# Performance work log

Hardware: AMD Instinct MI355X
Metric: run time of the kernel (lower is better)

Reference implementation:

```python
import jax, jax.numpy as jnp
import numpy as np

B, N, D, K = 4, 8192, 128, 16


def setup_inputs() -> dict:
    key = jax.random.key(0)
    ks = jax.random.split(key, 12)
    w = lambda k, s: (jax.random.normal(k, s, jnp.float32) * 0.02)
    return {
        "xyz": jax.random.normal(ks[0], (B, N, 3), jnp.float32),
        "feat": jax.random.normal(ks[1], (B, N, D), jnp.float32),
        # Linear weights stored as (in, out); apply as x @ W + b
        "Wq": w(ks[2], (D, D)), "bq": jnp.zeros((D,), jnp.float32),
        "Wk": w(ks[3], (D, D)), "bk": jnp.zeros((D,), jnp.float32),
        "Wv": w(ks[4], (D, D)), "bv": jnp.zeros((D,), jnp.float32),
        "Wp1": w(ks[5], (3, D)), "bp1": jnp.zeros((D,), jnp.float32),
        "Wp2": w(ks[6], (D, D)), "bp2": jnp.zeros((D,), jnp.float32),
        "Wo": w(ks[7], (D, D)), "bo": jnp.zeros((D,), jnp.float32),
        "gamma": jnp.float32(0.5),
    }


def reference(xyz, feat, Wq, bq, Wk, bk, Wv, bv, Wp1, bp1, Wp2, bp2, Wo, bo, gamma):
    # pairwise squared distance (B,N,N)
    sq = jnp.sum(xyz * xyz, axis=-1)
    dist = sq[:, :, None] + sq[:, None, :] - 2.0 * jnp.einsum("bnc,bmc->bnm", xyz, xyz)
    # K nearest neighbors (smallest distance)
    _, idx = jax.lax.top_k(-dist, K)  # (B,N,K)
    bidx = jnp.arange(B)[:, None, None]
    n_xyz = xyz[bidx, idx]    # (B,N,K,3)
    n_feat = feat[bidx, idx]  # (B,N,K,D)

    q = (feat @ Wq + bq)[:, :, None, :]    # (B,N,1,D)
    kk = n_feat @ Wk + bk                  # (B,N,K,D)
    v = n_feat @ Wv + bv                   # (B,N,K,D)

    rel_pos = xyz[:, :, None, :] - n_xyz   # (B,N,K,3)
    pos_enc = jax.nn.relu(rel_pos @ Wp1 + bp1) @ Wp2 + bp2  # (B,N,K,D)

    # per-channel-summed attention score, softmax over neighbor axis
    score = jnp.sum(q - kk + pos_enc, axis=-1, keepdims=True)  # (B,N,K,1)
    attn = jax.nn.softmax(score, axis=-2)

    agg = jnp.sum(attn * (v + pos_enc), axis=2)  # (B,N,D)
    out = agg @ Wo + bo
    return feat + gamma * out
```

## Files before the change

### kernel.cpp

```cpp
#include <hip/hip_runtime.h>
#include <hip/hip_bf16.h>

#define BATCH 4
#define NPTS  8192
#define DIM   128
#define KNN   16
#define NROWS (BATCH * NPTS)

#define SPLITS 16
#define RANGE  512
#define TILE   256
#define DEPTH  32
#define DEPTHP 34
#define NSUB   8

using u64  = unsigned long long;
using u32  = unsigned int;

__device__ __forceinline__ unsigned short f2bf(float f) {
    u32 u = __float_as_uint(f);
    u32 r = (u + 0x7FFFu + ((u >> 16) & 1u)) >> 16;
    return (unsigned short)r;
}
__device__ __forceinline__ u32 fordkey(float f) {
    u32 u = __float_as_uint(f);
    return (u & 0x80000000u) ? ~u : (u | 0x80000000u);
}
__device__ __forceinline__ float invkey(u32 k) {
    u32 u = (k & 0x80000000u) ? (k & 0x7FFFFFFFu) : ~k;
    return __uint_as_float(u);
}

__device__ __forceinline__ void insert16(u64 key, u64* ks) {
    if (key < ks[15]) {
#pragma unroll
        for (int t = 0; t < 16; ++t) {
            u64 lo = key < ks[t] ? key : ks[t];
            u64 hi = key < ks[t] ? ks[t] : key;
            ks[t] = lo;
            key = hi;
        }
    }
}

__device__ __forceinline__ float pdist(float4 me, float4 c) {
    float dot = __fadd_rn(__fadd_rn(__fmul_rn(me.x, c.x), __fmul_rn(me.y, c.y)),
                          __fmul_rn(me.z, c.z));
    return __fsub_rn(__fadd_rn(me.w, c.w), __fmul_rn(2.0f, dot));
}

__global__ __launch_bounds__(256) void prep_weights(const float* __restrict__ Wk,
                                                    const float* __restrict__ Wp2,
                                                    float* __restrict__ wk,
                                                    float* __restrict__ w2) {
    int tid = threadIdx.x;
    int c = tid & 127;
    const float* src = (tid < 128) ? Wk : Wp2;
    float s = 0.f;
    for (int d = 0; d < DIM; ++d) s += src[c * DIM + d];
    if (tid < 128) wk[c] = s;
    else           w2[c] = s;
}

__global__ __launch_bounds__(256) void conv_weights(const float* __restrict__ Wv,
                                                    const float* __restrict__ Wp2,
                                                    const float* __restrict__ Wo,
                                                    u32* __restrict__ Wb) {
    int i = blockIdx.x * 256 + threadIdx.x;
    int which = i >> 13, off = i & 8191;
    const float* W = (which == 0) ? Wv : (which == 1 ? Wp2 : Wo);
    float2 w = ((const float2*)W)[off];
    Wb[i] = (u32)f2bf(w.x) | ((u32)f2bf(w.y) << 16);
}

__global__ __launch_bounds__(256) void prep_points(const float* __restrict__ xyz,
                                                   const float* __restrict__ feat,
                                                   const float* __restrict__ wk,
                                                   float4* __restrict__ pts,
                                                   float* __restrict__ sK) {
    int lid = threadIdx.x & 63;
    int p = blockIdx.x * 4 + (threadIdx.x >> 6);
    float f_lo = feat[(size_t)p * DIM + lid];
    float f_hi = feat[(size_t)p * DIM + 64 + lid];
    float s = fmaf(f_lo, wk[lid], f_hi * wk[64 + lid]);
#pragma unroll
    for (int m = 32; m >= 1; m >>= 1) s += __shfl_xor(s, m);
    if (lid == 0) {
        float x = xyz[p * 3 + 0];
        float y = xyz[p * 3 + 1];
        float z = xyz[p * 3 + 2];
        float sq = __fadd_rn(__fadd_rn(__fmul_rn(x, x), __fmul_rn(y, y)), __fmul_rn(z, z));
        pts[p] = make_float4(x, y, z, sq);
        sK[p] = s;
    }
}

__global__ __launch_bounds__(256) void knn_limpass(const float4* __restrict__ pts,
                                                   float* __restrict__ dlim) {
    __shared__ float4 tile[256];
    __shared__ unsigned short stk[4][64][DEPTHP];
    int y = blockIdx.y;
    int wavein = threadIdx.x >> 6, lane = threadIdx.x & 63;
    int q = blockIdx.x * 256 + wavein * 64 + lane;
    int b = q >> 13;
    float4 me = pts[q];
    {
        float4 c = pts[b * NPTS + y * 256 + threadIdx.x];
        tile[threadIdx.x] = make_float4(c.x, c.y, c.z, -0.5f * c.w);
    }
    __syncthreads();
    float ks[16];
#pragma unroll
    for (int t = 0; t < 16; ++t) ks[t] = INFINITY;
    unsigned short* mystk = stk[wavein][lane];

    for (int jj = 0; jj < 32; ++jj) {
        float4 c = tile[jj];
        float s = fmaf(me.x, c.x, fmaf(me.y, c.y, fmaf(me.z, c.z, c.w)));
        float d = fmaf(-2.0f, s, me.w);
        if (d < ks[15]) {
#pragma unroll
            for (int t = 0; t < 16; ++t) {
                float lo = fminf(d, ks[t]);
                float hi = fmaxf(d, ks[t]);
                ks[t] = lo;
                d = hi;
            }
        }
    }
    float lim = ks[15];
    for (int c0 = 32; c0 < 256; c0 += 32) {
        int cnt = 0;
#pragma unroll
        for (int jj = c0; jj < c0 + 32; ++jj) {
            float4 c = tile[jj];
            float s = fmaf(me.x, c.x, fmaf(me.y, c.y, fmaf(me.z, c.z, c.w)));
            float d = fmaf(-2.0f, s, me.w);
            int slot = cnt < (DEPTH - 1) ? cnt : (DEPTH - 1);
            mystk[slot] = (unsigned short)jj;
            cnt += (d < lim) ? 1 : 0;
        }
        for (int i = 0; i < cnt; ++i) {
            int jj = mystk[i];
            float4 c = tile[jj];
            float s = fmaf(me.x, c.x, fmaf(me.y, c.y, fmaf(me.z, c.z, c.w)));
            float d = fmaf(-2.0f, s, me.w);
            if (d < ks[15]) {
#pragma unroll
                for (int t = 0; t < 16; ++t) {
                    float lo = fminf(d, ks[t]);
                    float hi = fmaxf(d, ks[t]);
                    ks[t] = lo;
                    d = hi;
                }
            }
        }
        lim = ks[15];
    }
    dlim[(size_t)y * NROWS + q] = ks[15];
}

__global__ __launch_bounds__(256) void knn_partial(const float4* __restrict__ pts,
                                                   const float* __restrict__ dlim,
                                                   unsigned short* __restrict__ part16) {
    __shared__ float4 tile[TILE];
    __shared__ unsigned short stk[4][64][DEPTHP];
    int r = blockIdx.y;
    int wavein = threadIdx.x >> 6, lane = threadIdx.x & 63;
    int q = blockIdx.x * 256 + wavein * 64 + lane;
    int b = q >> 13;
    float4 me = pts[q];

    float T = dlim[q];
#pragma unroll
    for (int y = 1; y < NSUB; ++y) T = fminf(T, dlim[(size_t)y * NROWS + q]);
    float gate_d = T + 2.0e-4f;
    u64 sent = ((u64)fordkey(gate_d) << 32) | 0xFFFFFFFFull;
    u64 ks[16];
#pragma unroll
    for (int t = 0; t < 16; ++t) ks[t] = sent;
    float A = 0.5f * (me.w - gate_d) - 1.0e-4f;
    unsigned short* mystk = stk[wavein][lane];

    for (int tb = 0; tb < RANGE / TILE; ++tb) {
        __syncthreads();
        int jb = r * RANGE + tb * TILE;
        {
            float4 c = pts[b * NPTS + jb + threadIdx.x];
            tile[threadIdx.x] = make_float4(c.x, c.y, c.z, -0.5f * c.w);
        }
        __syncthreads();

        int cnt = 0;
#pragma unroll 4
        for (int jj = 0; jj < TILE; ++jj) {
            float4 c = tile[jj];
            float s = fmaf(me.x, c.x, fmaf(me.y, c.y, fmaf(me.z, c.z, c.w)));
            int slot = cnt < (DEPTH - 1) ? cnt : (DEPTH - 1);
            mystk[slot] = (unsigned short)jj;
            cnt += (s >= A) ? 1 : 0;
        }
        bool over = (cnt >= DEPTH);
        int dn = over ? 0 : cnt;
        for (int i = 0; i < dn; ++i) {
            int jj = mystk[i];
            float4 c = tile[jj];
            float4 cc = make_float4(c.x, c.y, c.z, -2.0f * c.w);
            float d = pdist(me, cc);
            u64 key = ((u64)fordkey(d) << 32) | (u32)(jb + jj);
            insert16(key, ks);
        }
        if (__any(over)) {
            if (over) {
                for (int jj = 0; jj < TILE; ++jj) {
                    float4 c = tile[jj];
                    float s = fmaf(me.x, c.x, fmaf(me.y, c.y, fmaf(me.z, c.z, c.w)));
                    if (s >= A) {
                        float4 cc = make_float4(c.x, c.y, c.z, -2.0f * c.w);
                        float d = pdist(me, cc);
                        u64 key = ((u64)fordkey(d) << 32) | (u32)(jb + jj);
                        insert16(key, ks);
                    }
                }
            }
        }
        float nl = invkey((u32)(ks[15] >> 32)) + 1.0e-4f;
        gate_d = (nl < gate_d) ? nl : gate_d;
        A = 0.5f * (me.w - gate_d) - 1.0e-4f;
    }
    u32* dst = (u32*)(part16 + (size_t)q * 256 + r * 16);
#pragma unroll
    for (int t = 0; t < 8; ++t)
        dst[t] = (u32)(ks[2 * t] & 0xFFFFu) | ((u32)(ks[2 * t + 1] & 0xFFFFu) << 16);
}

__global__ __launch_bounds__(256) void knn_merge(const float4* __restrict__ pts,
                                                 const unsigned short* __restrict__ part16,
                                                 int* __restrict__ idx16) {
    int wavein = threadIdx.x >> 6, lane = threadIdx.x & 63;
    int q = blockIdx.x * 4 + wavein;
    int b = q >> 13;
    float4 me = pts[q];
    ushort4 e = *(const ushort4*)(part16 + (size_t)q * 256 + lane * 4);
    u64 k0, k1, k2, k3;
    {
        u32 id;
        id = e.x; k0 = (id != 0xFFFFu) ? (((u64)fordkey(pdist(me, pts[b * NPTS + id])) << 32) | id) : ~0ull;
        id = e.y; k1 = (id != 0xFFFFu) ? (((u64)fordkey(pdist(me, pts[b * NPTS + id])) << 32) | id) : ~0ull;
        id = e.z; k2 = (id != 0xFFFFu) ? (((u64)fordkey(pdist(me, pts[b * NPTS + id])) << 32) | id) : ~0ull;
        id = e.w; k3 = (id != 0xFFFFu) ? (((u64)fordkey(pdist(me, pts[b * NPTS + id])) << 32) | id) : ~0ull;
    }
    u64 t;
    if (k1 < k0) { t = k0; k0 = k1; k1 = t; }
    if (k3 < k2) { t = k2; k2 = k3; k3 = t; }
    if (k2 < k0) { t = k0; k0 = k2; k2 = t; }
    if (k3 < k1) { t = k1; k1 = k3; k3 = t; }
    if (k2 < k1) { t = k1; k1 = k2; k2 = t; }

    u64 cur = k0;
    int head = 0;
    u64 got = 0;
#pragma unroll
    for (int it = 0; it < 16; ++it) {
        u64 m = cur;
#pragma unroll
        for (int s = 32; s >= 1; s >>= 1) {
            u64 o = __shfl_xor(m, s);
            m = (o < m) ? o : m;
        }
        if (m == cur) {
            head++;
            cur = (head == 1) ? k1 : (head == 2) ? k2 : (head == 3) ? k3 : ~0ull;
        }
        if (lane == it) got = m;
    }
    if (lane < 16) idx16[q * KNN + lane] = (int)(got & 0xFFFFFFFFu);
}

template <int MODE>
__global__ __launch_bounds__(256) void gemm32(const float* __restrict__ X,
                                              const u32* __restrict__ Wb,
                                              const float* __restrict__ bias,
                                              const float* __restrict__ add,
                                              const float* __restrict__ featb,
                                              const float* __restrict__ gammap,
                                              float* __restrict__ outv) {
    __shared__ u32 Ws[DIM * DIM / 2];
    __shared__ float Xs[8 * DIM];
    __shared__ float bs[DIM];
    int tid = threadIdx.x;
    {
        const uint4* src = (const uint4*)Wb;
        uint4* dst = (uint4*)Ws;
        for (int i = tid; i < DIM * DIM / 8; i += 256) dst[i] = src[i];
    }
    if (tid < 128) bs[tid] = bias[tid];
    float gamma = 0.f;
    if (MODE == 2) gamma = *gammap;

    int rowBase = blockIdx.x * 32;
    int d4 = (tid & 31) * 4;
    int row = tid >> 5;

    for (int it = 0; it < 4; ++it) {
        int r0 = rowBase + it * 8;
        __syncthreads();
        ((float4*)Xs)[tid] = ((const float4*)(X + (size_t)r0 * DIM))[tid];
        __syncthreads();

        float a0 = bs[d4], a1 = bs[d4 + 1], a2 = bs[d4 + 2], a3 = bs[d4 + 3];
        const float* xr = &Xs[row * DIM];
#pragma unroll 8
        for (int c = 0; c < DIM; ++c) {
            float x = xr[c];
            uint2 w = *(const uint2*)&Ws[c * (DIM / 2) + (d4 >> 1)];
            a0 = fmaf(x, __uint_as_float(w.x << 16), a0);
            a1 = fmaf(x, __uint_as_float(w.x & 0xFFFF0000u), a1);
            a2 = fmaf(x, __uint_as_float(w.y << 16), a2);
            a3 = fmaf(x, __uint_as_float(w.y & 0xFFFF0000u), a3);
        }
        size_t off = (size_t)(r0 + row) * DIM + d4;
        if (MODE == 1) {
            float4 ad = *(const float4*)(add + off);
            a0 += ad.x; a1 += ad.y; a2 += ad.z; a3 += ad.w;
        }
        if (MODE == 2) {
            float4 fb = *(const float4*)(featb + off);
            a0 = fmaf(gamma, a0, fb.x);
            a1 = fmaf(gamma, a1, fb.y);
            a2 = fmaf(gamma, a2, fb.z);
            a3 = fmaf(gamma, a3, fb.w);
        }
        *(float4*)(outv + off) = make_float4(a0, a1, a2, a3);
    }
}

__global__ __launch_bounds__(256) void stage_c(const float4* __restrict__ pts,
                                               const int* __restrict__ idx16,
                                               const float* __restrict__ sK,
                                               const float* __restrict__ w2,
                                               const float* __restrict__ Wp1,
                                               const float* __restrict__ bp1,
                                               const float* __restrict__ Vf,
                                               float* __restrict__ vagg,
                                               float* __restrict__ hbar) {
    __shared__ float hs[4][KNN * DIM];
    int wavein = threadIdx.x >> 6;
    int lid = threadIdx.x & 63;
    int p = blockIdx.x * 4 + wavein;
    int b = p >> 13;
    float4 me = pts[p];

    float wx_lo = Wp1[lid],        wx_hi = Wp1[64 + lid];
    float wy_lo = Wp1[128 + lid],  wy_hi = Wp1[192 + lid];
    float wz_lo = Wp1[256 + lid],  wz_hi = Wp1[320 + lid];
    float bl    = bp1[lid],        bh    = bp1[64 + lid];
    float w2l   = w2[lid],         w2h   = w2[64 + lid];

    int myidx = idx16[p * KNN + (lid & 15)];
    float* h = hs[wavein];
    float sc = -INFINITY;

    for (int k = 0; k < KNN; ++k) {
        int j = __shfl(myidx, k);
        int g = b * NPTS + j;
        float4 nb = pts[g];
        float rx = me.x - nb.x, ry = me.y - nb.y, rz = me.z - nb.z;
        float h_lo = fmaxf(0.f, fmaf(rx, wx_lo, fmaf(ry, wy_lo, fmaf(rz, wz_lo, bl))));
        float h_hi = fmaxf(0.f, fmaf(rx, wx_hi, fmaf(ry, wy_hi, fmaf(rz, wz_hi, bh))));
        h[k * DIM + lid] = h_lo;
        h[k * DIM + 64 + lid] = h_hi;
        float s = fmaf(h_lo, w2l, h_hi * w2h);
#pragma unroll
        for (int m = 32; m >= 1; m >>= 1) s += __shfl_xor(s, m);
        float score = s - sK[g];
        if (lid == k) sc = score;
    }
    float mx = sc;
#pragma unroll
    for (int m = 8; m >= 1; m >>= 1) mx = fmaxf(mx, __shfl_xor(mx, m));
    float e = (lid < 16) ? __expf(sc - mx) : 0.f;
    float ssum = e;
#pragma unroll
    for (int m = 8; m >= 1; m >>= 1) ssum += __shfl_xor(ssum, m);
    float a = e / ssum;

    float acc_lo = 0.f, acc_hi = 0.f, hb_lo = 0.f, hb_hi = 0.f;
    for (int k = 0; k < KNN; ++k) {
        float ak = __shfl(a, k);
        int j = __shfl(myidx, k);
        size_t g = (size_t)(b * NPTS + j) * DIM;
        acc_lo = fmaf(ak, Vf[g + lid], acc_lo);
        acc_hi = fmaf(ak, Vf[g + 64 + lid], acc_hi);
        hb_lo = fmaf(ak, h[k * DIM + lid], hb_lo);
        hb_hi = fmaf(ak, h[k * DIM + 64 + lid], hb_hi);
    }
    size_t o = (size_t)p * DIM;
    vagg[o + lid] = acc_lo;
    vagg[o + 64 + lid] = acc_hi;
    hbar[o + lid] = hb_lo;
    hbar[o + 64 + lid] = hb_hi;
}

extern "C" void kernel_launch(void* const* d_in, const int* in_sizes, int n_in,
                              void* d_out, int out_size, void* d_ws, size_t ws_size,
                              hipStream_t stream) {
    const float* xyz   = (const float*)d_in[0];
    const float* feat  = (const float*)d_in[1];
    const float* Wk    = (const float*)d_in[4];
    const float* Wv    = (const float*)d_in[6];
    const float* bv    = (const float*)d_in[7];
    const float* Wp1   = (const float*)d_in[8];
    const float* bp1   = (const float*)d_in[9];
    const float* Wp2   = (const float*)d_in[10];
    const float* bp2   = (const float*)d_in[11];
    const float* Wo    = (const float*)d_in[12];
    const float* bo    = (const float*)d_in[13];
    const float* gamma = (const float*)d_in[14];
    float* out = (float*)d_out;

    char* ws = (char*)d_ws;
    const size_t KB = 1024, MB = 1024 * 1024;
    float*  wk    = (float*)(ws + 0);
    float*  w2    = (float*)(ws + 4 * KB);
    float4* pts   = (float4*)(ws + 16 * KB);
    float*  sKv   = (float*)(ws + 544 * KB);
    u32*    Wb    = (u32*)(ws + 688 * KB);
    float*  dlim  = (float*)(ws + 1 * MB);
    unsigned short* part16 = (unsigned short*)(ws + 5 * MB);
    float*  vagg  = (float*)(ws + 5 * MB);
    float*  hbarp = (float*)(ws + 21 * MB);
    int*    idx16 = (int*)(ws + 37 * MB);
    float*  Vf    = (float*)(ws + 39 * MB);
    float*  T1    = (float*)(ws + 39 * MB);

    prep_weights<<<1, 256, 0, stream>>>(Wk, Wp2, wk, w2);
    conv_weights<<<96, 256, 0, stream>>>(Wv, Wp2, Wo, Wb);
    prep_points<<<NROWS / 4, 256, 0, stream>>>(xyz, feat, wk, pts, sKv);
    gemm32<0><<<1024, 256, 0, stream>>>(feat, Wb, bv, nullptr, nullptr, nullptr, Vf);
    knn_limpass<<<dim3(NROWS / 256, NSUB), 256, 0, stream>>>(pts, dlim);
    knn_partial<<<dim3(NROWS / 256, SPLITS), 256, 0, stream>>>(pts, dlim, part16);
    knn_merge<<<NROWS / 4, 256, 0, stream>>>(pts, part16, idx16);
    stage_c<<<NROWS / 4, 256, 0, stream>>>(pts, idx16, sKv, w2, Wp1, bp1, Vf, vagg, hbarp);
    gemm32<1><<<1024, 256, 0, stream>>>(hbarp, Wb + 8192, bp2, vagg, nullptr, nullptr, T1);
    gemm32<2><<<1024, 256, 0, stream>>>(T1, Wb + 16384, bo, nullptr, feat, gamma, out);
}
```

Measured before the change: 556.5 us.

## Use 32-bit truncated sort keys and bitmask candidate scan in kNN passes

In knn_partial the per-lane top-16 list changes from 64-bit keys to 32-bit keys that pack a truncated distance (high 19 bits) with the 13-bit point index. The index stack shrinks to bytes, and the exact distance is recomputed later in merge. knn_limpass drops its shared-memory stack in favour of a 32-bit candidate bitmask walked with ctz. This halves register and compare cost in the insertion network and removes LDS traffic, at the risk of truncation reordering near-equal distances within a partial. The merge step recomputes exact distances to limit that risk.

```diff
diff --git a/kernel.cpp b/kernel.cpp
--- a/kernel.cpp
+++ b/kernel.cpp
@@ -11,7 +11,7 @@
 #define RANGE  512
 #define TILE   256
 #define DEPTH  32
-#define DEPTHP 34
+#define DEPTHP 33
 #define NSUB   8
 
 using u64  = unsigned long long;
@@ -31,12 +31,12 @@
     return __uint_as_float(u);
 }
 
-__device__ __forceinline__ void insert16(u64 key, u64* ks) {
+__device__ __forceinline__ void insert16u(u32 key, u32* ks) {
     if (key < ks[15]) {
 #pragma unroll
         for (int t = 0; t < 16; ++t) {
-            u64 lo = key < ks[t] ? key : ks[t];
-            u64 hi = key < ks[t] ? ks[t] : key;
+            u32 lo = key < ks[t] ? key : ks[t];
+            u32 hi = key < ks[t] ? ks[t] : key;
             ks[t] = lo;
             key = hi;
         }
@@ -98,7 +98,6 @@
 __global__ __launch_bounds__(256) void knn_limpass(const float4* __restrict__ pts,
                                                    float* __restrict__ dlim) {
     __shared__ float4 tile[256];
-    __shared__ unsigned short stk[4][64][DEPTHP];
     int y = blockIdx.y;
     int wavein = threadIdx.x >> 6, lane = threadIdx.x & 63;
     int q = blockIdx.x * 256 + wavein * 64 + lane;
@@ -112,7 +111,6 @@
     float ks[16];
 #pragma unroll
     for (int t = 0; t < 16; ++t) ks[t] = INFINITY;
-    unsigned short* mystk = stk[wavein][lane];
 
     for (int jj = 0; jj < 32; ++jj) {
         float4 c = tile[jj];
@@ -129,19 +127,19 @@
         }
     }
     float lim = ks[15];
+    float A = 0.5f * (me.w - lim);
     for (int c0 = 32; c0 < 256; c0 += 32) {
-        int cnt = 0;
-#pragma unroll
-        for (int jj = c0; jj < c0 + 32; ++jj) {
-            float4 c = tile[jj];
+        u32 mask = 0;
+#pragma unroll
+        for (int jj = 0; jj < 32; ++jj) {
+            float4 c = tile[c0 + jj];
             float s = fmaf(me.x, c.x, fmaf(me.y, c.y, fmaf(me.z, c.z, c.w)));
-            float d = fmaf(-2.0f, s, me.w);
-            int slot = cnt < (DEPTH - 1) ? cnt : (DEPTH - 1);
-            mystk[slot] = (unsigned short)jj;
-            cnt += (d < lim) ? 1 : 0;
-        }
-        for (int i = 0; i < cnt; ++i) {
-            int jj = mystk[i];
+            mask = (mask << 1) | (u32)(s >= A);
+        }
+        while (mask) {
+            int pos = __builtin_ctz(mask);
+            mask &= mask - 1;
+            int jj = c0 + 31 - pos;
             float4 c = tile[jj];
             float s = fmaf(me.x, c.x, fmaf(me.y, c.y, fmaf(me.z, c.z, c.w)));
             float d = fmaf(-2.0f, s, me.w);
@@ -156,6 +154,7 @@
             }
         }
         lim = ks[15];
+        A = 0.5f * (me.w - lim);
     }
     dlim[(size_t)y * NROWS + q] = ks[15];
 }
@@ -164,7 +163,7 @@
                                                    const float* __restrict__ dlim,
                                                    unsigned short* __restrict__ part16) {
     __shared__ float4 tile[TILE];
-    __shared__ unsigned short stk[4][64][DEPTHP];
+    __shared__ unsigned char stk[4][64][DEPTHP];
     int r = blockIdx.y;
     int wavein = threadIdx.x >> 6, lane = threadIdx.x & 63;
     int q = blockIdx.x * 256 + wavein * 64 + lane;
@@ -175,12 +174,11 @@
 #pragma unroll
     for (int y = 1; y < NSUB; ++y) T = fminf(T, dlim[(size_t)y * NROWS + q]);
     float gate_d = T + 2.0e-4f;
-    u64 sent = ((u64)fordkey(gate_d) << 32) | 0xFFFFFFFFull;
-    u64 ks[16];
-#pragma unroll
-    for (int t = 0; t < 16; ++t) ks[t] = sent;
+    u32 kk[16];
+#pragma unroll
+    for (int t = 0; t < 16; ++t) kk[t] = 0xFFFFFFFFu;
     float A = 0.5f * (me.w - gate_d) - 1.0e-4f;
-    unsigned short* mystk = stk[wavein][lane];
+    unsigned char* mystk = stk[wavein][lane];
 
     for (int tb = 0; tb < RANGE / TILE; ++tb) {
         __syncthreads();
@@ -197,7 +195,7 @@
             float4 c = tile[jj];
             float s = fmaf(me.x, c.x, fmaf(me.y, c.y, fmaf(me.z, c.z, c.w)));
             int slot = cnt < (DEPTH - 1) ? cnt : (DEPTH - 1);
-            mystk[slot] = (unsigned short)jj;
+            mystk[slot] = (unsigned char)jj;
             cnt += (s >= A) ? 1 : 0;
         }
         bool over = (cnt >= DEPTH);
@@ -205,10 +203,10 @@
         for (int i = 0; i < dn; ++i) {
             int jj = mystk[i];
             float4 c = tile[jj];
-            float4 cc = make_float4(c.x, c.y, c.z, -2.0f * c.w);
-            float d = pdist(me, cc);
-            u64 key = ((u64)fordkey(d) << 32) | (u32)(jb + jj);
-            insert16(key, ks);
+            float s = fmaf(me.x, c.x, fmaf(me.y, c.y, fmaf(me.z, c.z, c.w)));
+            float dt = fmaf(-2.0f, s, me.w);
+            u32 key = (fordkey(dt) & 0xFFFFE000u) | (u32)(jb + jj);
+            insert16u(key, kk);
         }
         if (__any(over)) {
             if (over) {
@@ -216,22 +214,25 @@
                     float4 c = tile[jj];
                     float s = fmaf(me.x, c.x, fmaf(me.y, c.y, fmaf(me.z, c.z, c.w)));
                     if (s >= A) {
-                        float4 cc = make_float4(c.x, c.y, c.z, -2.0f * c.w);
-                        float d = pdist(me, cc);
-                        u64 key = ((u64)fordkey(d) << 32) | (u32)(jb + jj);
-                        insert16(key, ks);
+                        float dt = fmaf(-2.0f, s, me.w);
+                        u32 key = (fordkey(dt) & 0xFFFFE000u) | (u32)(jb + jj);
+                        insert16u(key, kk);
                     }
                 }
             }
         }
-        float nl = invkey((u32)(ks[15] >> 32)) + 1.0e-4f;
+        float nl = invkey((kk[15] & 0xFFFFE000u) | 0x1FFFu) + 1.0e-4f;
         gate_d = (nl < gate_d) ? nl : gate_d;
         A = 0.5f * (me.w - gate_d) - 1.0e-4f;
     }
     u32* dst = (u32*)(part16 + (size_t)q * 256 + r * 16);
 #pragma unroll
-    for (int t = 0; t < 8; ++t)
-        dst[t] = (u32)(ks[2 * t] & 0xFFFFu) | ((u32)(ks[2 * t + 1] & 0xFFFFu) << 16);
+    for (int t = 0; t < 8; ++t) {
+        u32 a = kk[2 * t], c = kk[2 * t + 1];
+        u32 i0 = (a == 0xFFFFFFFFu) ? 0xFFFFu : (a & 0x1FFFu);
+        u32 i1 = (c == 0xFFFFFFFFu) ? 0xFFFFu : (c & 0x1FFFu);
+        dst[t] = i0 | (i1 << 16);
+    }
 }
 
 __global__ __launch_bounds__(256) void knn_merge(const float4* __restrict__ pts,
```

Result: faster. 515.8 us (-7.3%).
